# Kernel optimization log

Hardware: AMD Instinct MI355X
Metric: run time of the kernel (lower is better)

## Reference

```python
import jax, jax.numpy as jnp
import numpy as np

EPS = float(np.finfo(np.float32).eps)
B, N, NUM_ATOM, K = 16, 256, 64, 20
NUM_EDGETYPE = 3
SHORT = (1, 2, 3)
LONG = (3, 5, 7)
HIDDEN = (128, 128)
OUT = 1
SCALES = len(SHORT) + len(LONG) + NUM_EDGETYPE + 1  # 10
LB = 1e-4  # lanczos breakdown tolerance


def _xavier(k, fi, fo):
    return jax.random.uniform(k, (fi, fo), jnp.float32, -1.0, 1.0) * (6.0 / (fi + fo)) ** 0.5


def setup_inputs() -> dict:
    key = jax.random.key(0)
    ks = jax.random.split(key, 12)
    inp = {}
    inp["node_feat"] = jax.random.randint(ks[0], (B, N), 0, NUM_ATOM)
    inp["L"] = jax.random.uniform(ks[1], (B, N, N, NUM_EDGETYPE + 1), jnp.float32)
    # embedding_map: Linear(num_atom,1024) -> ReLU -> Linear(1024,num_atom)
    inp["emb_w1"] = _xavier(ks[2], NUM_ATOM, 1024); inp["emb_b1"] = jnp.zeros((1024,), jnp.float32)
    inp["emb_w2"] = _xavier(ks[3], 1024, NUM_ATOM); inp["emb_b2"] = jnp.zeros((NUM_ATOM,), jnp.float32)
    # eigen_map per long scale: Linear(K*K,1024) -> ReLU -> Linear(1024,K*K)
    S, K2 = len(LONG), K * K
    inp["eig_w1"] = jnp.stack([_xavier(jax.random.fold_in(ks[4], i), K2, 1024) for i in range(S)])
    inp["eig_b1"] = jnp.zeros((S, 1024), jnp.float32)
    inp["eig_w2"] = jnp.stack([_xavier(jax.random.fold_in(ks[5], i), 1024, K2) for i in range(S)])
    inp["eig_b2"] = jnp.zeros((S, K2), jnp.float32)
    dims = [NUM_ATOM] + list(HIDDEN) + [OUT]
    inp["filt_w0"] = _xavier(ks[6], dims[0] * SCALES, dims[1]); inp["filt_b0"] = jnp.zeros((dims[1],), jnp.float32)
    inp["filt_w1"] = _xavier(ks[7], dims[1] * SCALES, dims[2]); inp["filt_b1"] = jnp.zeros((dims[2],), jnp.float32)
    inp["filt_wo"] = _xavier(ks[8], dims[2], dims[3]); inp["filt_bo"] = jnp.zeros((dims[3],), jnp.float32)
    inp["att_w"] = _xavier(ks[9], dims[2], 1); inp["att_b"] = jnp.zeros((1,), jnp.float32)
    return inp


def _graph_laplacian(feat, adj_mask):
    # feat: B x N x D; pairwise gaussian affinity, sym-normalized (alpha=0.5)
    diff = feat[:, :, None, :] - feat[:, None, :, :]           # B,N,N,D
    dist2 = jnp.sum(diff * diff, axis=-1).reshape(B, -1)       # B,N*N
    sigma2 = jnp.mean(dist2, axis=1, keepdims=True)
    A = jnp.exp(-dist2 / sigma2).reshape(B, N, N) * adj_mask
    row_sum = jnp.sum(A, axis=2, keepdims=True)
    pad = jnp.where(row_sum == 0.0, 1.0, 0.0)
    D = 1.0 / jnp.sqrt(row_sum + pad)
    return D * A * jnp.swapaxes(D, 1, 2)


def _lanczos(A, key):
    # sequential Lanczos tridiagonalization with double Gram-Schmidt reorth
    q = jax.random.normal(key, (B, N), jnp.float32)
    q = q / jnp.linalg.norm(q, axis=1, keepdims=True)

    def step(carry, i):
        Qbuf, q_prev, qc, beta_prev, valid = carry
        z = jnp.einsum('bij,bj->bi', A, qc)
        alpha = jnp.sum(qc * z, axis=1)
        z = z - alpha[:, None] * qc - beta_prev[:, None] * q_prev
        for _ in range(2):  # reorthogonalize against Q[1..ii-1] (zero cols are no-ops)
            coef = jnp.einsum('bnk,bn->bk', Qbuf, z) / (jnp.sum(Qbuf * Qbuf, axis=1) + EPS)
            z = z - jnp.einsum('bnk,bk->bn', Qbuf, coef)
        beta = jnp.sqrt(jnp.sum(z * z, axis=1))
        valid = valid * (beta >= LB).astype(jnp.float32)
        q_next = z * valid[:, None] / (beta[:, None] + EPS)
        Qbuf = Qbuf.at[:, :, i].set(qc)
        return (Qbuf, qc, q_next, beta, valid), (alpha, beta, valid, qc)

    init = (jnp.zeros((B, N, K), jnp.float32), jnp.zeros((B, N), jnp.float32), q,
            jnp.zeros((B,), jnp.float32), jnp.ones((B,), jnp.float32))
    _, (alphas, betas, valids, qs) = jax.lax.scan(step, init, jnp.arange(K))
    alpha = alphas.T            # B,K
    beta = betas.T              # B,K
    valid = valids.T            # B,K (cumulative 1..1 0..0)
    idx = jnp.sum(valid, axis=1).astype(jnp.int32)   # rank per sample
    alpha = alpha * valid
    beta = beta[:, :K - 1] * valid[:, :K - 1]
    T = jax.vmap(lambda a, b: jnp.diag(a) + jnp.diag(b, 1) + jnp.diag(b, -1))(alpha, beta)
    Q = jnp.transpose(qs, (1, 2, 0))  # B,N,K
    # faithful to source: zero node rows >= idx_mask (only when idx < N)
    row_ok = (jnp.arange(N)[None, :] < idx[:, None]) | (idx[:, None] >= N)
    Q = Q * valid[:, None, :] * row_ok[:, :, None].astype(jnp.float32)
    return T, Q


def _spectral_filters(T, Q, eig_w1, eig_b1, eig_w2, eig_b2, key):
    T_list = []
    TT = T
    b = jax.random.normal(key, (B, K, 1), jnp.float32)
    Tb = b / jnp.linalg.norm(b, axis=1, keepdims=True)
    for ii in range(max(LONG) + 1):
        if ii in LONG:
            T_list.append(TT)
        TT = TT @ T
        # power-iteration cap on spectral radius
        Tb_new = T @ Tb
        l_max = jnp.sum(Tb_new * Tb, axis=1, keepdims=True) / (jnp.sum(Tb * Tb, axis=1, keepdims=True) + EPS)
        TT = TT * (jnp.abs(l_max) <= 1.0).astype(jnp.float32)
        Tb = Tb_new / (jnp.linalg.norm(Tb_new, axis=1, keepdims=True) + EPS)
    triu = jnp.triu(jnp.ones((K, K), jnp.float32))
    eye = jnp.eye(K, dtype=jnp.float32)
    outs = []
    for s in range(len(LONG)):
        h = jax.nn.relu(T_list[s].reshape(B, -1) @ eig_w1[s] + eig_b1[s])
        DD = (h @ eig_w2[s] + eig_b2[s]).reshape(B, K, K)
        DD = DD * triu
        DD = DD + jnp.swapaxes(DD, 1, 2) * (1.0 - eye)  # symmetrize
        outs.append(jnp.einsum('bnk,bkl,bml->bnm', Q, DD, Q))
    return jnp.stack(outs, axis=3)  # B,N,N,S


def reference(node_feat, L, emb_w1, emb_b1, emb_w2, emb_b2, eig_w1, eig_b1, eig_w2, eig_b2,
              filt_w0, filt_b0, filt_w1, filt_b1, filt_wo, filt_bo, att_w, att_b):
    key = jax.random.key(42)
    state = jax.nn.one_hot(node_feat, NUM_ATOM, dtype=jnp.float32)  # frozen identity embedding
    feat = jax.nn.relu(state @ emb_w1 + emb_b1) @ emb_w2 + emb_b2
    Lk = _graph_laplacian(feat, L[:, :, :, 0])
    T, Q = _lanczos(Lk, jax.random.fold_in(key, 0))
    filt_w = (filt_w0, filt_w1)
    filt_b = (filt_b0, filt_b1)
    for tt in range(len(HIDDEN)):
        msg = []
        DD = _spectral_filters(T, Q, eig_w1, eig_b1, eig_w2, eig_b2, jax.random.fold_in(key, tt + 1))
        tmp = state
        for ii in range(1, max(SHORT) + 1):  # short diffusion
            tmp = jnp.einsum('bij,bjd->bid', Lk, tmp)
            if ii in SHORT:
                msg.append(tmp)
        for s in range(len(LONG)):           # long (spectral) diffusion
            msg.append(jnp.einsum('bij,bjd->bid', DD[:, :, :, s], state))
        for e in range(NUM_EDGETYPE + 1):     # per-edgetype propagation
            msg.append(jnp.einsum('bij,bjd->bid', L[:, :, :, e], state))
        msg = jnp.concatenate(msg, axis=2)    # B,N,10*D
        state = jax.nn.relu(msg @ filt_w[tt] + filt_b[tt])
    y = state @ filt_wo + filt_bo             # B,N,1
    att = jax.nn.sigmoid(state @ att_w + att_b)
    score = jnp.mean(att * y, axis=1)          # B,OUT (mask=None -> mean over nodes)
    return score
```

## Files before the change

### kernel.cpp

```cpp
#include <hip/hip_runtime.h>


constexpr int nB = 16;
constexpr int nN = 256;
constexpr int nK = 20;
constexpr int QS = nN + 1;
constexpr float EPSF = 1.1920928955078125e-07f;
constexpr float LBF  = 1e-4f;

#define DEV static __device__ __forceinline__

DEV void tf2x32(unsigned k0, unsigned k1, unsigned x0, unsigned x1,
                unsigned &o0, unsigned &o1) {
  unsigned ks2 = k0 ^ k1 ^ 0x1BD11BDAu;
#define RND(r) { x0 += x1; x1 = (x1 << r) | (x1 >> (32 - r)); x1 ^= x0; }
  x0 += k0;  x1 += k1;
  RND(13) RND(15) RND(26) RND(6)
  x0 += k1;  x1 += ks2 + 1u;
  RND(17) RND(29) RND(16) RND(24)
  x0 += ks2; x1 += k0 + 2u;
  RND(13) RND(15) RND(26) RND(6)
  x0 += k0;  x1 += k1 + 3u;
  RND(17) RND(29) RND(16) RND(24)
  x0 += k1;  x1 += ks2 + 4u;
  RND(13) RND(15) RND(26) RND(6)
  x0 += ks2; x1 += k0 + 5u;
#undef RND
  o0 = x0; o1 = x1;
}

DEV float erfinv_f32(float x) {
  float w = -log1pf(-x * x);
  float p;
  if (w < 5.0f) {
    w -= 2.5f;
    p = 2.81022636e-08f;
    p = fmaf(p, w, 3.43273939e-07f);
    p = fmaf(p, w, -3.5233877e-06f);
    p = fmaf(p, w, -4.39150654e-06f);
    p = fmaf(p, w, 0.00021858087f);
    p = fmaf(p, w, -0.00125372503f);
    p = fmaf(p, w, -0.00417768164f);
    p = fmaf(p, w, 0.246640727f);
    p = fmaf(p, w, 1.50140941f);
  } else {
    w = sqrtf(w) - 3.0f;
    p = -0.000200214257f;
    p = fmaf(p, w, 0.000100950558f);
    p = fmaf(p, w, 0.00134934322f);
    p = fmaf(p, w, -0.00367342844f);
    p = fmaf(p, w, 0.00573950773f);
    p = fmaf(p, w, -0.0076224613f);
    p = fmaf(p, w, 0.00943887047f);
    p = fmaf(p, w, 1.00167406f);
    p = fmaf(p, w, 2.83297682f);
  }
  return p * x;
}

DEV float jax_normal(unsigned k0, unsigned k1, unsigned idx) {
  unsigned o0, o1;
  tf2x32(k0, k1, 0u , idx , o0, o1);
  unsigned bits = o0 ^ o1;
  float u = __uint_as_float((bits >> 9) | 0x3f800000u) - 1.0f;
  const float lo = -0.99999994f;
  float v = fmaxf(lo, u * 2.0f + lo);
  return 1.41421356237309515f * erfinv_f32(v);
}

DEV double waveRedD(double v) {
#pragma unroll
  for (int m = 32; m > 0; m >>= 1) v += __shfl_xor(v, m, 64);
  return v;
}
DEV float waveRedF(float v) {
#pragma unroll
  for (int m = 32; m > 0; m >>= 1) v += __shfl_xor(v, m, 64);
  return v;
}
DEV double blockSumD(double v, double *s4) {
  v = waveRedD(v);
  int w = threadIdx.x >> 6;
  __syncthreads();
  if ((threadIdx.x & 63) == 0) s4[w] = v;
  __syncthreads();
  return s4[0] + s4[1] + s4[2] + s4[3];
}
DEV double sum8(const double *r) {
  return ((r[0] + r[1]) + (r[2] + r[3])) + ((r[4] + r[5]) + (r[6] + r[7]));
}

__global__ __launch_bounds__(256) void feat_table_kernel(
    const float *__restrict__ w1, const float *__restrict__ b1,
    const float *__restrict__ w2, const float *__restrict__ b2,
    float *__restrict__ table) {
  int a = blockIdx.x, t = threadIdx.x;
  __shared__ float hh[1024];
  __shared__ float part[256];
  for (int k = t; k < 1024; k += 256)
    hh[k] = fmaxf(w1[(size_t)a * 1024 + k] + b1[k], 0.f);
  __syncthreads();
  int d = t & 63, slice = t >> 6;
  float acc = 0.f;
  for (int k = slice * 256; k < slice * 256 + 256; k++)
    acc += hh[k] * w2[(size_t)k * 64 + d];
  part[t] = acc;
  __syncthreads();
  if (t < 64)
    table[(size_t)a * 64 + t] =
        part[t] + part[64 + t] + part[128 + t] + part[192 + t] + b2[t];
}

__global__ __launch_bounds__(256) void feat_state_tr_kernel(
    const int *__restrict__ nf, const float *__restrict__ table,
    float *__restrict__ feat, float *__restrict__ featT,
    float *__restrict__ state0) {
  int g = blockIdx.x;
  int bb = g >> 2, n0 = (g & 3) * 64;
  int t = threadIdx.x;
  int c = t & 63, r4 = t >> 6;
  __shared__ float tl[64][65];
  __shared__ int av[64];
  if (t < 64) av[t] = nf[bb * nN + n0 + t];
  __syncthreads();
  for (int r = r4; r < 64; r += 4) {
    int a = av[r];
    float v = table[(size_t)a * 64 + c];
    tl[r][c] = v;
    feat[((size_t)(bb * nN + n0 + r)) * 64 + c] = v;
    state0[((size_t)(bb * nN + n0 + r)) * 64 + c] = (c == a) ? 1.f : 0.f;
  }
  __syncthreads();
  for (int r = r4; r < 64; r += 4)
    featT[(size_t)bb * 16384 + (size_t)r * nN + n0 + c] = tl[c][r];
}

__global__ __launch_bounds__(256) void dist2_kernel(
    const float *__restrict__ feat, const float *__restrict__ featT,
    float *__restrict__ G, double *__restrict__ part) {
  int g = blockIdx.x;
  int bb = g >> 6, i0 = (g & 63) * 4;
  int t = threadIdx.x;
  __shared__ float fi[4][64];
  __shared__ double s4[4];
  {
    int r = t >> 6, d = t & 63;
    fi[r][d] = feat[((size_t)(bb * nN + i0 + r)) * 64 + d];
  }
  __syncthreads();
  const float *ft = featT + (size_t)bb * 16384 + t;
  float a0 = 0.f, a1 = 0.f, a2 = 0.f, a3 = 0.f;
#pragma unroll 8
  for (int d = 0; d < 64; d++) {
    float x = ft[(size_t)d * nN];
    float d0 = fi[0][d] - x; a0 += d0 * d0;
    float d1 = fi[1][d] - x; a1 += d1 * d1;
    float d2 = fi[2][d] - x; a2 += d2 * d2;
    float d3 = fi[3][d] - x; a3 += d3 * d3;
  }
  size_t base = ((size_t)bb * nN + i0) * nN + t;
  G[base]           = a0;
  G[base + nN]      = a1;
  G[base + 2 * nN]  = a2;
  G[base + 3 * nN]  = a3;
  double tot = blockSumD((double)a0 + (double)a1 + (double)a2 + (double)a3, s4);
  if (t == 0) part[g] = tot;
}

__global__ __launch_bounds__(256) void arow_kernel(
    const float *__restrict__ Lfull, const double *__restrict__ part,
    float *__restrict__ G, float *__restrict__ Dv) {
  int g = blockIdx.x;
  int i = g % nN, bb = g / nN;
  int t = threadIdx.x;
  __shared__ double s4[4];
  __shared__ float ssig;
  if (t < 64) {
    double v = part[(size_t)bb * 64 + t];
    v = waveRedD(v);
    if (t == 0) ssig = (float)(v / 65536.0);
  }
  __syncthreads();
  float sig = ssig;
  size_t idx2 = ((size_t)bb * nN + i) * nN + t;
  float a = expf(-G[idx2] / sig) * Lfull[idx2 * 4];
  G[idx2] = a;
  double rs = blockSumD((double)a, s4);
  if (t == 0) {
    float r = (float)rs;
    float pad = (r == 0.f) ? 1.f : 0.f;
    Dv[(size_t)bb * nN + i] = 1.f / sqrtf(r + pad);
  }
}

__global__ __launch_bounds__(256) void lkscale_tr_kernel(
    float *__restrict__ G, const float *__restrict__ Dv,
    float *__restrict__ GT) {
  int g = blockIdx.x;
  int bb = g >> 4, tile = g & 15;
  int ti = (tile >> 2) * 64, tj = (tile & 3) * 64;
  int t = threadIdx.x;
  int lj = t & 63, li0 = t >> 6;
  __shared__ float tl[64][65];
  for (int r = li0; r < 64; r += 4) {
    int i = ti + r;
    size_t idx = ((size_t)bb * nN + i) * nN + tj + lj;
    float v = Dv[(size_t)bb * nN + i] * G[idx] * Dv[(size_t)bb * nN + tj + lj];
    G[idx] = v;
    tl[r][lj] = v;
  }
  __syncthreads();
  for (int r = li0; r < 64; r += 4) {
    int j = tj + r;
    GT[((size_t)bb * nN + j) * nN + ti + lj] = tl[lj][r];
  }
}

__global__ __launch_bounds__(512)
void lanczos_kernel(const float *__restrict__ GT, float *__restrict__ Qout,
                    float *__restrict__ Tout) {
  __shared__ float Qb[nK * QS];
  __shared__ float qc[nN], qp[nN], zz[nN];
  __shared__ double zp[2][nN];
  __shared__ float qn2[nK], sAl[nK], sBe[nK], sVa[nK], coef[nK];
  __shared__ double redA[8], redB[8];
  int bb = blockIdx.x, u = threadIdx.x;
  int t = u & 255, h = u >> 8;
  int wv = u >> 6, lane = u & 63;
  int gid = u >> 4, gl = u & 15;

  const float *Gcol = GT + (size_t)bb * (nN * nN) + (size_t)(h * 128) * nN + t;

  unsigned k0, k1;
  tf2x32(0u, 42u, 0u, 0u, k0, k1);
  float val = 0.f;
  if (h == 0) val = jax_normal(k0, k1, (unsigned)(bb * nN + t));
  {
    double v = waveRedD((double)val * (double)val);
    __syncthreads();
    if (lane == 0) redA[wv] = v;
    __syncthreads();
    double n2 = sum8(redA);
    if (h == 0) {
      qc[t] = val / sqrtf((float)n2);
      qp[t] = 0.f;
    }
  }
  __syncthreads();

  float beta_prev = 0.f, validf = 1.f;

  for (int i = 0; i < nK; i++) {
    double a0 = 0, a1 = 0, a2 = 0, a3 = 0, a4 = 0, a5 = 0, a6 = 0, a7 = 0;
    {
      const float *qv = qc + h * 128;
#pragma unroll
      for (int jj = 0; jj < 128; jj += 8) {
        a0 += (double)Gcol[(size_t)(jj + 0) * nN] * (double)qv[jj + 0];
        a1 += (double)Gcol[(size_t)(jj + 1) * nN] * (double)qv[jj + 1];
        a2 += (double)Gcol[(size_t)(jj + 2) * nN] * (double)qv[jj + 2];
        a3 += (double)Gcol[(size_t)(jj + 3) * nN] * (double)qv[jj + 3];
        a4 += (double)Gcol[(size_t)(jj + 4) * nN] * (double)qv[jj + 4];
        a5 += (double)Gcol[(size_t)(jj + 5) * nN] * (double)qv[jj + 5];
        a6 += (double)Gcol[(size_t)(jj + 6) * nN] * (double)qv[jj + 6];
        a7 += (double)Gcol[(size_t)(jj + 7) * nN] * (double)qv[jj + 7];
      }
    }
    double part = ((a0 + a1) + (a2 + a3)) + ((a4 + a5) + (a6 + a7));
    zp[h][t] = part;
    double apart = (double)qc[t] * part;
    double qpart = (h == 0) ? (double)qc[t] * (double)qc[t] : 0.0;
    apart = waveRedD(apart);
    qpart = waveRedD(qpart);
    if (lane == 0) { redA[wv] = apart; redB[wv] = qpart; }
    __syncthreads();
    float alpha = (float)sum8(redA);
    if (h == 0) {
      float zi = (float)(zp[0][t] + zp[1][t]);
      zi = zi - alpha * qc[t] - beta_prev * qp[t];
      zz[t] = zi;
    } else {
      Qb[i * QS + t] = qc[t];
      if (t == 0) qn2[i] = (float)sum8(redB);
    }
    __syncthreads();
    if (gid < i) {
      double p = 0.0;
#pragma unroll
      for (int j = 0; j < 16; j++) {
        int n0 = gl + 16 * j;
        p += (double)Qb[gid * QS + n0] * (double)zz[n0];
      }
#pragma unroll
      for (int m = 1; m <= 8; m <<= 1) p += __shfl_xor(p, m, 64);
      if (gl == 0)
        coef[gid] = (float)(p / ((double)qn2[gid] + (double)EPSF));
    }
    __syncthreads();
    if (h == 0) {
      double sub = 0.0;
      for (int k = 0; k < i; k++)
        sub += (double)Qb[k * QS + t] * (double)coef[k];
      zz[t] = (float)((double)zz[t] - sub);
    }
    __syncthreads();
    if (gid < i) {
      double p = 0.0;
#pragma unroll
      for (int j = 0; j < 16; j++) {
        int n0 = gl + 16 * j;
        p += (double)Qb[gid * QS + n0] * (double)zz[n0];
      }
#pragma unroll
      for (int m = 1; m <= 8; m <<= 1) p += __shfl_xor(p, m, 64);
      if (gl == 0)
        coef[gid] = (float)(p / ((double)qn2[gid] + (double)EPSF));
    }
    __syncthreads();
    double bpart = 0.0;
    if (h == 0) {
      double sub = 0.0;
      for (int k = 0; k < i; k++)
        sub += (double)Qb[k * QS + t] * (double)coef[k];
      float znew = (float)((double)zz[t] - sub);
      zz[t] = znew;
      bpart = (double)znew * (double)znew;
    }
    bpart = waveRedD(bpart);
    if (lane == 0) redA[wv] = bpart;
    __syncthreads();
    float beta = sqrtf((float)sum8(redA));
    validf *= (beta >= LBF) ? 1.f : 0.f;
    if (u == 0) {
      sAl[i] = alpha;
      sBe[i] = beta;
      sVa[i] = validf;
    }
    if (h == 0) {
      float qnext = zz[t] * validf / (beta + EPSF);
      qp[t] = qc[t];
      qc[t] = qnext;
    }
    __syncthreads();
    beta_prev = beta;
  }

  float idxf = 0.f;
  for (int k = 0; k < nK; k++) idxf += sVa[k];
  int idx = (int)idxf;
  if (h == 0) {
    float rowok = ((t < idx) || (idx >= nN)) ? 1.f : 0.f;
    for (int k = 0; k < nK; k++)
      Qout[((size_t)bb * nN + t) * nK + k] = Qb[k * QS + t] * sVa[k] * rowok;
  }
  for (int e = u; e < nK * nK; e += 512) {
    int i = e / nK, j = e % nK;
    float v = 0.f;
    if (i == j) v = sAl[i] * sVa[i];
    else if (j == i + 1) v = sBe[i] * sVa[i];
    else if (i == j + 1) v = sBe[j] * sVa[j];
    Tout[(size_t)bb * nK * nK + e] = v;
  }
}

DEV void spect_body(const float *__restrict__ Tin, float *__restrict__ Tpow2,
                    int bb, int tt, int t, char *smem) {
  float *T_  = (float *)smem;
  float *TT  = T_ + nK * nK;
  float *TTn = TT + nK * nK;
  float *Tb  = TTn + nK * nK;
  float *Tbn = Tb + nK;
  for (int e = t; e < nK * nK; e += 64) {
    float v = Tin[(size_t)bb * nK * nK + e];
    T_[e] = v;
    TT[e] = v;
  }
  unsigned k0, k1;
  tf2x32(0u, 42u, 0u, (unsigned)(tt + 1), k0, k1);
  if (t < nK) Tb[t] = jax_normal(k0, k1, (unsigned)(bb * nK + t));
  __syncthreads();
  float pv = (t < nK) ? Tb[t] * Tb[t] : 0.f;
  float nb = sqrtf(waveRedF(pv));
  if (t < nK) Tb[t] = Tb[t] / nb;
  __syncthreads();
  for (int ii = 0; ii < 8; ii++) {
    if (ii == 3 || ii == 5 || ii == 7) {
      int s = (ii - 3) / 2;
      int sf = tt * 3 + s;
      for (int e = t; e < nK * nK; e += 64)
        Tpow2[((size_t)sf * nB + bb) * nK * nK + e] = TT[e];
    }
    __syncthreads();
    for (int e = t; e < nK * nK; e += 64) {
      int i = e / nK, j = e % nK;
      float a = 0.f;
      for (int l = 0; l < nK; l++) a += TT[i * nK + l] * T_[l * nK + j];
      TTn[e] = a;
    }
    if (t < nK) {
      float a = 0.f;
      for (int l = 0; l < nK; l++) a += T_[t * nK + l] * Tb[l];
      Tbn[t] = a;
    }
    __syncthreads();
    float pn = (t < nK) ? Tbn[t] * Tb[t] : 0.f;
    float pd = (t < nK) ? Tb[t] * Tb[t] : 0.f;
    float num = waveRedF(pn);
    float den = waveRedF(pd);
    float lmax = num / (den + EPSF);
    float keep = (fabsf(lmax) <= 1.0f) ? 1.f : 0.f;
    __syncthreads();
    for (int e = t; e < nK * nK; e += 64) TT[e] = TTn[e] * keep;
    float p2 = (t < nK) ? Tbn[t] * Tbn[t] : 0.f;
    float nn = sqrtf(waveRedF(p2));
    if (t < nK) Tb[t] = Tbn[t] / (nn + EPSF);
    __syncthreads();
  }
}

DEV void eig1_body(const float *__restrict__ Tpow2, const float *__restrict__ w1p,
                   const float *__restrict__ b1p, float *__restrict__ h2,
                   int g, int t, char *smem) {
  int oc = g & 15, sf = g >> 4;
  int sw = sf % 3;
  int o = (t & 63) + oc * 64, bbg = t >> 6;
  float *tp = (float *)smem;
  for (int e = t; e < nB * 400; e += 256)
    tp[e] = Tpow2[(size_t)sf * nB * 400 + e];
  __syncthreads();
  float bias = b1p[(size_t)sw * 1024 + o];
  float acc0 = bias, acc1 = bias, acc2 = bias, acc3 = bias;
  const float *W = w1p + (size_t)sw * 400 * 1024 + o;
  const float *t0 = tp + (bbg + 0) * 400;
  const float *t1 = tp + (bbg + 4) * 400;
  const float *t2 = tp + (bbg + 8) * 400;
  const float *t3 = tp + (bbg + 12) * 400;
  for (int k = 0; k < 400; k++) {
    float w = W[(size_t)k * 1024];
    acc0 += t0[k] * w;
    acc1 += t1[k] * w;
    acc2 += t2[k] * w;
    acc3 += t3[k] * w;
  }
  h2[((size_t)sf * nB + (bbg + 0))  * 1024 + o] = fmaxf(acc0, 0.f);
  h2[((size_t)sf * nB + (bbg + 4))  * 1024 + o] = fmaxf(acc1, 0.f);
  h2[((size_t)sf * nB + (bbg + 8))  * 1024 + o] = fmaxf(acc2, 0.f);
  h2[((size_t)sf * nB + (bbg + 12)) * 1024 + o] = fmaxf(acc3, 0.f);
}

DEV void eig2_body(const float *__restrict__ h2, const float *__restrict__ w2p,
                   const float *__restrict__ b2p, float *__restrict__ raw2,
                   int g, int t, char *smem) {
  int kc = g % 25, sf = g / 25;
  int sw = sf % 3;
  int kl = (t & 15) + kc * 16, bb = t >> 4;
  float *hh = (float *)smem;
  for (int e = t; e < nB * 1024; e += 256)
    hh[(e >> 10) * 1025 + (e & 1023)] = h2[(size_t)sf * nB * 1024 + e];
  __syncthreads();
  float acc = b2p[(size_t)sw * 400 + kl];
  const float *W = w2p + (size_t)sw * 1024 * 400 + kl;
  const float *hv = hh + bb * 1025;
  for (int o = 0; o < 1024; o++) acc += hv[o] * W[(size_t)o * 400];
  raw2[((size_t)sf * nB + bb) * 400 + kl] = acc;
}

DEV void qtstate_body(const float *__restrict__ Q, const float *__restrict__ state,
                      float *__restrict__ E, int g, int t, int Din, char *smem) {
  int k = g % nK, bb = g / nK;
  float *qcol = (float *)smem;
  for (int n = t; n < nN; n += Din)
    qcol[n] = Q[((size_t)bb * nN + n) * nK + k];
  __syncthreads();
  const float *st = state + (size_t)bb * nN * Din;
  float acc = 0.f;
  for (int n = 0; n < nN; n++) acc += qcol[n] * st[(size_t)n * Din + t];
  E[((size_t)bb * nK + k) * Din + t] = acc;
}

DEV void lk_body(const float *__restrict__ Lk, const float *__restrict__ in,
                 int inStride, float *__restrict__ out, int outStride,
                 int g, int t, int Din, char *smem) {
  int bb = g >> 5, r0 = (g & 31) * 8;
  float (*rows)[nN] = (float (*)[nN])smem;
  for (int e = t; e < 8 * nN; e += Din) {
    int r = e >> 8, j = e & 255;
    rows[r][j] = Lk[((size_t)bb * nN + r0 + r) * nN + j];
  }
  __syncthreads();
  float acc[8] = {0.f, 0.f, 0.f, 0.f, 0.f, 0.f, 0.f, 0.f};
  const float *ip = in + (size_t)bb * nN * inStride + t;
  for (int j = 0; j < nN; j++) {
    float x = ip[(size_t)j * inStride];
#pragma unroll
    for (int r = 0; r < 8; r++) acc[r] += rows[r][j] * x;
  }
#pragma unroll
  for (int r = 0; r < 8; r++)
    out[((size_t)bb * nN + r0 + r) * outStride + t] = acc[r];
}

DEV void edgemsg_body(const float *__restrict__ Lfull,
                      const float *__restrict__ state, float *__restrict__ msg,
                      int C, int g, int t, int Din, char *smem) {
  int bb = g >> 6, r0 = (g & 63) * 4;
  float4 (*rows4)[nN] = (float4 (*)[nN])smem;
  const float4 *L4 = (const float4 *)Lfull;
  for (int e = t; e < 4 * nN; e += Din) {
    int r = e >> 8, j = e & 255;
    rows4[r][j] = L4[((size_t)bb * nN + r0 + r) * nN + j];
  }
  __syncthreads();
  float acc[4][4];
#pragma unroll
  for (int r = 0; r < 4; r++)
#pragma unroll
    for (int e = 0; e < 4; e++) acc[r][e] = 0.f;
  const float *st = state + (size_t)bb * nN * Din + t;
  for (int j = 0; j < nN; j++) {
    float x = st[(size_t)j * Din];
#pragma unroll
    for (int r = 0; r < 4; r++) {
      float4 lv = rows4[r][j];
      acc[r][0] += lv.x * x;
      acc[r][1] += lv.y * x;
      acc[r][2] += lv.z * x;
      acc[r][3] += lv.w * x;
    }
  }
#pragma unroll
  for (int r = 0; r < 4; r++)
#pragma unroll
    for (int e = 0; e < 4; e++)
      msg[((size_t)bb * nN + r0 + r) * C + (6 + e) * Din + t] = acc[r][e];
}

DEV void ddE_body(const float *__restrict__ raw, const float *__restrict__ E,
                  float *__restrict__ F, int g, int t, int Din, char *smem) {
  int k = g % nK, bb = (g / nK) % nB, s = g / (nK * nB);
  float *dr = (float *)smem;
  if (t < nK) {
    int mi = k < t ? k : t, ma = k < t ? t : k;
    dr[t] = raw[((size_t)s * nB + bb) * 400 + mi * nK + ma];
  }
  __syncthreads();
  float acc = 0.f;
  for (int l = 0; l < nK; l++)
    acc += dr[l] * E[((size_t)bb * nK + l) * Din + t];
  F[(((size_t)s * nB + bb) * nK + k) * Din + t] = acc;
}

DEV void longmsg_body(const float *__restrict__ Q, const float *__restrict__ F,
                      float *__restrict__ msg, int C, int g, int t, int Din,
                      char *smem) {
  int i = g % nN, bb = g / nN;
  float *qr = (float *)smem;
  if (t < nK) qr[t] = Q[((size_t)bb * nN + i) * nK + t];
  __syncthreads();
  for (int s = 0; s < 3; s++) {
    float acc = 0.f;
    for (int k = 0; k < nK; k++)
      acc += qr[k] * F[(((size_t)s * nB + bb) * nK + k) * Din + t];
    msg[((size_t)bb * nN + i) * C + (3 + s) * Din + t] = acc;
  }
}

__global__ __launch_bounds__(64) void l1d1_spect_kernel(
    const float *__restrict__ T, float *__restrict__ Tpow2) {
  __shared__ __align__(16) char smem[5120];
  int bb = blockIdx.x & 15, tt = blockIdx.x >> 4;
  spect_body(T, Tpow2, bb, tt, threadIdx.x, smem);
}

__global__ void msgD1_kernel(const float *__restrict__ Q,
                             const float *__restrict__ state,
                             float *__restrict__ E,
                             const float *__restrict__ Lk,
                             float *__restrict__ msg,
                             const float *__restrict__ Lfull, int C) {
  __shared__ __align__(16) char smem[16384];
  int t = threadIdx.x, Din = blockDim.x;
  int gb = blockIdx.x;
  if (gb < nB * nK) {
    qtstate_body(Q, state, E, gb, t, Din, smem);
  } else if (gb < nB * nK + nB * nN / 8) {
    lk_body(Lk, state, Din, msg + 0 * Din, C, gb - nB * nK, t, Din, smem);
  } else {
    edgemsg_body(Lfull, state, msg, C, gb - nB * nK - nB * nN / 8, t, Din, smem);
  }
}

__global__ __launch_bounds__(256) void l1d2_kernel(
    const float *__restrict__ Tpow2, const float *__restrict__ w1p,
    const float *__restrict__ b1p, float *__restrict__ h2,
    const float *__restrict__ Lk, float *__restrict__ msg, int C) {
  __shared__ __align__(16) char smem[26240];
  int t = threadIdx.x;
  int gb = blockIdx.x;
  if (gb < 96) {
    eig1_body(Tpow2, w1p, b1p, h2, gb, t, smem);
  } else {
    int g = gb - 96;
    int bb = g >> 5, r0 = (g & 31) * 8;
    float (*rows)[nN] = (float (*)[nN])smem;
    for (int e = t; e < 8 * nN; e += 256) {
      int r = e >> 8, j = e & 255;
      rows[r][j] = Lk[((size_t)bb * nN + r0 + r) * nN + j];
    }
    __syncthreads();
    if (t < 64) {
      float acc[8] = {0.f, 0.f, 0.f, 0.f, 0.f, 0.f, 0.f, 0.f};
      const float *ip = msg + (size_t)bb * nN * C + 0 * 64 + t;
      for (int j = 0; j < nN; j++) {
        float x = ip[(size_t)j * C];
#pragma unroll
        for (int r = 0; r < 8; r++) acc[r] += rows[r][j] * x;
      }
#pragma unroll
      for (int r = 0; r < 8; r++)
        msg[((size_t)bb * nN + r0 + r) * C + 1 * 64 + t] = acc[r];
    }
  }
}

__global__ __launch_bounds__(256) void l1d3_kernel(
    const float *__restrict__ h2, const float *__restrict__ w2p,
    const float *__restrict__ b2p, float *__restrict__ raw2,
    const float *__restrict__ Lk, float *__restrict__ msg, int C) {
  __shared__ __align__(16) char smem[65600];
  int t = threadIdx.x;
  int gb = blockIdx.x;
  if (gb < 150) {
    eig2_body(h2, w2p, b2p, raw2, gb, t, smem);
  } else {
    int g = gb - 150;
    int bb = g >> 5, r0 = (g & 31) * 8;
    float (*rows)[nN] = (float (*)[nN])smem;
    for (int e = t; e < 8 * nN; e += 256) {
      int r = e >> 8, j = e & 255;
      rows[r][j] = Lk[((size_t)bb * nN + r0 + r) * nN + j];
    }
    __syncthreads();
    if (t < 64) {
      float acc[8] = {0.f, 0.f, 0.f, 0.f, 0.f, 0.f, 0.f, 0.f};
      const float *ip = msg + (size_t)bb * nN * C + 1 * 64 + t;
      for (int j = 0; j < nN; j++) {
        float x = ip[(size_t)j * C];
#pragma unroll
        for (int r = 0; r < 8; r++) acc[r] += rows[r][j] * x;
      }
#pragma unroll
      for (int r = 0; r < 8; r++)
        msg[((size_t)bb * nN + r0 + r) * C + 2 * 64 + t] = acc[r];
    }
  }
}

__global__ void msgD2_kernel(const float *__restrict__ raw,
                             const float *__restrict__ E,
                             float *__restrict__ F,
                             const float *__restrict__ Lk,
                             float *__restrict__ msg, int C, int withLk) {
  __shared__ __align__(16) char smem[8192];
  int t = threadIdx.x, Din = blockDim.x;
  int gb = blockIdx.x;
  if (gb < 3 * nB * nK) {
    ddE_body(raw, E, F, gb, t, Din, smem);
  } else {
    lk_body(Lk, msg + 0 * Din, C, msg + 1 * Din, C, gb - 3 * nB * nK, t, Din,
            smem);
  }
}

__global__ void msgD3_kernel(const float *__restrict__ Q,
                             const float *__restrict__ F,
                             const float *__restrict__ Lk,
                             float *__restrict__ msg, int C) {
  __shared__ __align__(16) char smem[8192];
  int t = threadIdx.x, Din = blockDim.x;
  int gb = blockIdx.x;
  if (gb < nB * nN) {
    longmsg_body(Q, F, msg, C, gb, t, Din, smem);
  } else {
    lk_body(Lk, msg + 1 * Din, C, msg + 2 * Din, C, gb - nB * nN, t, Din, smem);
  }
}

__global__ __launch_bounds__(256) void filt_kernel(
    const float *__restrict__ msg, const float *__restrict__ W,
    const float *__restrict__ bias, float *__restrict__ out, int C) {
  int g = blockIdx.x;
  int base = g * 16;
  int t = threadIdx.x;
  int o = t & 127, ih = t >> 7;
  __shared__ float mt[16][64];
  __shared__ float wt[64][128];
  float acc[8];
  float bo = bias[o];
#pragma unroll
  for (int r = 0; r < 8; r++) acc[r] = bo;
  for (int c0 = 0; c0 < C; c0 += 64) {
    __syncthreads();
    for (int e = t; e < 16 * 64; e += 256) {
      int r = e >> 6, c = e & 63;
      mt[r][c] = msg[((size_t)(base + r)) * C + c0 + c];
    }
    for (int e = t; e < 64 * 128; e += 256)
      wt[e >> 7][e & 127] = W[(size_t)(c0 + (e >> 7)) * 128 + (e & 127)];
    __syncthreads();
    for (int c = 0; c < 64; c++) {
      float w = wt[c][o];
#pragma unroll
      for (int r = 0; r < 8; r++) acc[r] += mt[ih * 8 + r][c] * w;
    }
  }
#pragma unroll
  for (int r = 0; r < 8; r++)
    out[((size_t)(base + ih * 8 + r)) * 128 + o] = fmaxf(acc[r], 0.f);
}

__global__ __launch_bounds__(256) void score_kernel(
    const float *__restrict__ state, const float *__restrict__ wo,
    const float *__restrict__ bo, const float *__restrict__ aw,
    const float *__restrict__ ab, float *__restrict__ out) {
  __shared__ float sl[64 * 129];
  __shared__ double s4[4];
  int bb = blockIdx.x, t = threadIdx.x;
  float bof = bo[0], abf = ab[0];
  double dsum = 0.0;
  for (int r0 = 0; r0 < nN; r0 += 64) {
    __syncthreads();
    for (int e = t; e < 64 * 128; e += 256) {
      int r = e >> 7, o = e & 127;
      sl[r * 129 + o] = state[((size_t)bb * nN + r0 + r) * 128 + o];
    }
    __syncthreads();
    if (t < 64) {
      const float *sr = sl + t * 129;
      float sy = bof, sa = abf;
      for (int o = 0; o < 128; o++) {
        float v = sr[o];
        sy += v * wo[o];
        sa += v * aw[o];
      }
      float att = 1.f / (1.f + expf(-sa));
      dsum += (double)(att * sy);
    }
  }
  double m = blockSumD(dsum, s4);
  if (t == 0) out[bb] = (float)(m / (double)nN);
}

extern "C" void kernel_launch(void *const *d_in, const int *in_sizes, int n_in,
                              void *d_out, int out_size, void *d_ws,
                              size_t ws_size, hipStream_t stream) {
  (void)in_sizes; (void)n_in; (void)out_size;
  const int   *node_feat = (const int *)d_in[0];
  const float *Lfull     = (const float *)d_in[1];
  const float *emb_w1    = (const float *)d_in[2];
  const float *emb_b1    = (const float *)d_in[3];
  const float *emb_w2    = (const float *)d_in[4];
  const float *emb_b2    = (const float *)d_in[5];
  const float *eig_w1    = (const float *)d_in[6];
  const float *eig_b1    = (const float *)d_in[7];
  const float *eig_w2    = (const float *)d_in[8];
  const float *eig_b2    = (const float *)d_in[9];
  const float *filt_w0   = (const float *)d_in[10];
  const float *filt_b0   = (const float *)d_in[11];
  const float *filt_w1   = (const float *)d_in[12];
  const float *filt_b1   = (const float *)d_in[13];
  const float *filt_wo   = (const float *)d_in[14];
  const float *filt_bo   = (const float *)d_in[15];
  const float *att_w     = (const float *)d_in[16];
  const float *att_b     = (const float *)d_in[17];

  float *ws   = (float *)d_ws;
  float *G    = ws;
  float *msg  = G + 1048576;
  float *st0  = msg + 5242880;
  float *st1  = st0 + 262144;
  float *st2  = st1 + 524288;
  float *feat = st2 + 524288;
  float *table= feat + 262144;
  float *Q    = table + 4096;
  float *T    = Q + 81920;
  float *Tpow = T + 6400;
  float *DD   = Tpow + 19200;
  float *h    = DD + 19200;
  float *E    = h + 49152;
  float *F    = E + 40960;
  float *Dv   = F + 122880;
  double *part   = (double *)(Dv + 4096);
  float *GT    = msg;
  float *featT = msg + 1048576;
  float *Tpow2 = feat;
  float *raw2  = feat + 38400;
  float *h2    = feat + 76800;
  const size_t needBytes = (size_t)(8220432) * 4;
  if (ws_size < needBytes) return;

  feat_table_kernel<<<64, 256, 0, stream>>>(emb_w1, emb_b1, emb_w2, emb_b2, table);
  feat_state_tr_kernel<<<nB * 4, 256, 0, stream>>>(node_feat, table, feat,
                                                   featT, st0);
  dist2_kernel<<<nB * 64, 256, 0, stream>>>(feat, featT, G, part);
  arow_kernel<<<nB * nN, 256, 0, stream>>>(Lfull, part, G, Dv);
  lkscale_tr_kernel<<<nB * 16, 256, 0, stream>>>(G, Dv, GT);
  lanczos_kernel<<<nB, 512, 0, stream>>>(GT, Q, T);

  const int QTB = nB * nK;
  const int LKB = nB * nN / 8;
  const int EDB = nB * nN / 4;
  const int DDB = 3 * nB * nK;
  const int LMB = nB * nN;

  {
    int Din = 64, C = 640;
    const float *rawT = raw2;
    l1d1_spect_kernel<<<nB * 2, 64, 0, stream>>>(T, Tpow2);
    msgD1_kernel<<<QTB + LKB + EDB, Din, 0, stream>>>(Q, st0, E, G, msg,
                                                      Lfull, C);
    l1d2_kernel<<<96 + LKB, 256, 0, stream>>>(Tpow2, eig_w1, eig_b1, h2, G,
                                              msg, C);
    l1d3_kernel<<<150 + LKB, 256, 0, stream>>>(h2, eig_w2, eig_b2, raw2, G,
                                               msg, C);
    msgD2_kernel<<<DDB, Din, 0, stream>>>(rawT, E, F, G, msg, C, 0);
    msgD3_kernel<<<LMB, Din, 0, stream>>>(Q, F, G, msg, C);
    filt_kernel<<<nB * nN / 16, 256, 0, stream>>>(msg, filt_w0, filt_b0, st1, C);
  }
  {
    int Din = 128, C = 1280;
    const float *rawT = raw2 + (size_t)3 * nB * 400;
    msgD1_kernel<<<QTB + LKB + EDB, Din, 0, stream>>>(Q, st1, E, G, msg,
                                                      Lfull, C);
    msgD2_kernel<<<DDB + LKB, Din, 0, stream>>>(rawT, E, F, G, msg, C, 1);
    msgD3_kernel<<<LMB + LKB, Din, 0, stream>>>(Q, F, G, msg, C);
    filt_kernel<<<nB * nN / 16, 256, 0, stream>>>(msg, filt_w1, filt_b1, st2, C);
  }
  score_kernel<<<nB, 256, 0, stream>>>(st2, filt_wo, filt_bo, att_w, att_b,
                                       (float *)d_out);
}
```

Baseline: 630.8 us.

## Overlap layer-1 Lk and edge-type messages with Lanczos; fold QtState into l1d2

Adds extra blocks to the Lanczos launch that compute the first short-diffusion product and the four edge-type propagations for layer 1. These can run on otherwise idle CUs while the 16 Lanczos blocks execute serially. The Q^T·state projection moves into the l1d2 kernel, which removes the separate msgD1 launch for layer 1. GT is relocated inside the msg buffer so the concurrent writes to msg do not overwrite it. The trade-off is that the Lanczos kernel now carries the shared-memory footprint of those extra blocks, and its blocks are scheduled alongside them.

```diff
diff --git a/kernel.cpp b/kernel.cpp
--- a/kernel.cpp
+++ b/kernel.cpp
@@ -218,14 +218,79 @@
 
 __global__ __launch_bounds__(512)
 void lanczos_kernel(const float *__restrict__ GT, float *__restrict__ Qout,
-                    float *__restrict__ Tout) {
+                    float *__restrict__ Tout, const float *__restrict__ state0,
+                    const float *__restrict__ Lfull, const float *__restrict__ G,
+                    float *__restrict__ msg) {
   __shared__ float Qb[nK * QS];
   __shared__ float qc[nN], qp[nN], zz[nN];
   __shared__ double zp[2][nN];
   __shared__ float qn2[nK], sAl[nK], sBe[nK], sVa[nK], coef[nK];
   __shared__ double redA[8], redB[8];
-  int bb = blockIdx.x, u = threadIdx.x;
-  int t = u & 255, h = u >> 8;
+  __shared__ __align__(16) char bsmem[16384];
+  int gb = blockIdx.x, u = threadIdx.x;
+
+  if (gb >= 16) {
+    const int C = 640;
+    if (gb < 16 + 512) {
+      int g = gb - 16;
+      int bb2 = g >> 5, r0 = (g & 31) * 8;
+      float (*rows)[nN] = (float (*)[nN])bsmem;
+      for (int e = u; e < 8 * nN; e += 512) {
+        int r = e >> 8, j = e & 255;
+        rows[r][j] = G[((size_t)bb2 * nN + r0 + r) * nN + j];
+      }
+      __syncthreads();
+      if (u < 64) {
+        float acc[8] = {0.f, 0.f, 0.f, 0.f, 0.f, 0.f, 0.f, 0.f};
+        const float *ip = state0 + (size_t)bb2 * nN * 64 + u;
+        for (int j = 0; j < nN; j++) {
+          float x = ip[(size_t)j * 64];
+#pragma unroll
+          for (int r = 0; r < 8; r++) acc[r] += rows[r][j] * x;
+        }
+#pragma unroll
+        for (int r = 0; r < 8; r++)
+          msg[((size_t)bb2 * nN + r0 + r) * C + 0 * 64 + u] = acc[r];
+      }
+    } else {
+      int g = gb - 528;
+      int bb2 = g >> 6, r0 = (g & 63) * 4;
+      float4 (*rows4)[nN] = (float4 (*)[nN])bsmem;
+      const float4 *L4 = (const float4 *)Lfull;
+      for (int e = u; e < 4 * nN; e += 512) {
+        int r = e >> 8, j = e & 255;
+        rows4[r][j] = L4[((size_t)bb2 * nN + r0 + r) * nN + j];
+      }
+      __syncthreads();
+      if (u < 64) {
+        float acc[4][4];
+#pragma unroll
+        for (int r = 0; r < 4; r++)
+#pragma unroll
+          for (int e = 0; e < 4; e++) acc[r][e] = 0.f;
+        const float *st = state0 + (size_t)bb2 * nN * 64 + u;
+        for (int j = 0; j < nN; j++) {
+          float x = st[(size_t)j * 64];
+#pragma unroll
+          for (int r = 0; r < 4; r++) {
+            float4 lv = rows4[r][j];
+            acc[r][0] += lv.x * x;
+            acc[r][1] += lv.y * x;
+            acc[r][2] += lv.z * x;
+            acc[r][3] += lv.w * x;
+          }
+        }
+#pragma unroll
+        for (int r = 0; r < 4; r++)
+#pragma unroll
+          for (int e = 0; e < 4; e++)
+            msg[((size_t)bb2 * nN + r0 + r) * C + (6 + e) * 64 + u] = acc[r][e];
+      }
+    }
+    return;
+  }
+
+  int bb = gb, t = u & 255, h = u >> 8;
   int wv = u >> 6, lane = u & 63;
   int gid = u >> 4, gl = u & 15;
 
@@ -572,35 +637,32 @@
   spect_body(T, Tpow2, bb, tt, threadIdx.x, smem);
 }
 
-__global__ void msgD1_kernel(const float *__restrict__ Q,
-                             const float *__restrict__ state,
-                             float *__restrict__ E,
-                             const float *__restrict__ Lk,
-                             float *__restrict__ msg,
-                             const float *__restrict__ Lfull, int C) {
-  __shared__ __align__(16) char smem[16384];
-  int t = threadIdx.x, Din = blockDim.x;
-  int gb = blockIdx.x;
-  if (gb < nB * nK) {
-    qtstate_body(Q, state, E, gb, t, Din, smem);
-  } else if (gb < nB * nK + nB * nN / 8) {
-    lk_body(Lk, state, Din, msg + 0 * Din, C, gb - nB * nK, t, Din, smem);
-  } else {
-    edgemsg_body(Lfull, state, msg, C, gb - nB * nK - nB * nN / 8, t, Din, smem);
-  }
-}
-
 __global__ __launch_bounds__(256) void l1d2_kernel(
     const float *__restrict__ Tpow2, const float *__restrict__ w1p,
     const float *__restrict__ b1p, float *__restrict__ h2,
-    const float *__restrict__ Lk, float *__restrict__ msg, int C) {
+    const float *__restrict__ Q, const float *__restrict__ state0,
+    float *__restrict__ E, const float *__restrict__ Lk,
+    float *__restrict__ msg, int C) {
   __shared__ __align__(16) char smem[26240];
   int t = threadIdx.x;
   int gb = blockIdx.x;
   if (gb < 96) {
     eig1_body(Tpow2, w1p, b1p, h2, gb, t, smem);
+  } else if (gb < 96 + 320) {
+    int g = gb - 96;
+    int k = g % nK, bb = g / nK;
+    float *qcol = (float *)smem;
+    for (int n = t; n < nN; n += 256)
+      qcol[n] = Q[((size_t)bb * nN + n) * nK + k];
+    __syncthreads();
+    if (t < 64) {
+      const float *st = state0 + (size_t)bb * nN * 64;
+      float acc = 0.f;
+      for (int n = 0; n < nN; n++) acc += qcol[n] * st[(size_t)n * 64 + t];
+      E[((size_t)bb * nK + k) * 64 + t] = acc;
+    }
   } else {
-    int g = gb - 96;
+    int g = gb - 416;
     int bb = g >> 5, r0 = (g & 31) * 8;
     float (*rows)[nN] = (float (*)[nN])smem;
     for (int e = t; e < 8 * nN; e += 256) {
@@ -653,6 +715,24 @@
       for (int r = 0; r < 8; r++)
         msg[((size_t)bb * nN + r0 + r) * C + 2 * 64 + t] = acc[r];
     }
+  }
+}
+
+__global__ void msgD1_kernel(const float *__restrict__ Q,
+                             const float *__restrict__ state,
+                             float *__restrict__ E,
+                             const float *__restrict__ Lk,
+                             float *__restrict__ msg,
+                             const float *__restrict__ Lfull, int C) {
+  __shared__ __align__(16) char smem[16384];
+  int t = threadIdx.x, Din = blockDim.x;
+  int gb = blockIdx.x;
+  if (gb < nB * nK) {
+    qtstate_body(Q, state, E, gb, t, Din, smem);
+  } else if (gb < nB * nK + nB * nN / 8) {
+    lk_body(Lk, state, Din, msg + 0 * Din, C, gb - nB * nK, t, Din, smem);
+  } else {
+    edgemsg_body(Lfull, state, msg, C, gb - nB * nK - nB * nN / 8, t, Din, smem);
   }
 }
 
@@ -791,7 +871,7 @@
   float *F    = E + 40960;
   float *Dv   = F + 122880;
   double *part   = (double *)(Dv + 4096);
-  float *GT    = msg;
+  float *GT    = msg + 4194304;
   float *featT = msg + 1048576;
   float *Tpow2 = feat;
   float *raw2  = feat + 38400;
@@ -805,7 +885,8 @@
   dist2_kernel<<<nB * 64, 256, 0, stream>>>(feat, featT, G, part);
   arow_kernel<<<nB * nN, 256, 0, stream>>>(Lfull, part, G, Dv);
   lkscale_tr_kernel<<<nB * 16, 256, 0, stream>>>(G, Dv, GT);
-  lanczos_kernel<<<nB, 512, 0, stream>>>(GT, Q, T);
+  lanczos_kernel<<<16 + 512 + 1024, 512, 0, stream>>>(GT, Q, T, st0, Lfull, G,
+                                                      msg);
 
   const int QTB = nB * nK;
   const int LKB = nB * nN / 8;
@@ -817,10 +898,8 @@
     int Din = 64, C = 640;
     const float *rawT = raw2;
     l1d1_spect_kernel<<<nB * 2, 64, 0, stream>>>(T, Tpow2);
-    msgD1_kernel<<<QTB + LKB + EDB, Din, 0, stream>>>(Q, st0, E, G, msg,
-                                                      Lfull, C);
-    l1d2_kernel<<<96 + LKB, 256, 0, stream>>>(Tpow2, eig_w1, eig_b1, h2, G,
-                                              msg, C);
+    l1d2_kernel<<<96 + QTB + LKB, 256, 0, stream>>>(Tpow2, eig_w1, eig_b1, h2,
+                                                    Q, st0, E, G, msg, C);
     l1d3_kernel<<<150 + LKB, 256, 0, stream>>>(h2, eig_w2, eig_b2, raw2, G,
                                                msg, C);
     msgD2_kernel<<<DDB, Din, 0, stream>>>(rawT, E, F, G, msg, C, 0);
```

After: 602.5 us. 4.5% less time.
